# Kernel tuning notes

Hardware: AMD Instinct MI355X
Metric: run time of the kernel (lower is better)

Reference implementation:

```python
import jax, jax.numpy as jnp
import numpy as np

EMBED_DIM = 256
NUM_HEADS = 8
HEAD_DIM = 32
INNER = NUM_HEADS * HEAD_DIM
NEG_SLOPE = 0.2


def setup_inputs() -> dict:
    key = jax.random.key(0)
    ks = jax.random.split(key, 8)
    B, Ns, Nt = 8, 1024, 1024
    src = jax.random.normal(ks[0], (B, Ns, EMBED_DIM), dtype=jnp.float32)
    trg = jax.random.normal(ks[1], (B, Nt, EMBED_DIM), dtype=jnp.float32)
    src_mask = jnp.ones((B, Ns), dtype=bool)
    trg_mask = jax.random.randint(ks[2], (B, Nt), 0, 2).astype(bool)
    # learned params (xavier-ish scale)
    def xavier(k, shape):
        fan_in, fan_out = shape[0], shape[-1]
        lim = (6.0 / (fan_in + fan_out)) ** 0.5
        return jax.random.uniform(k, shape, jnp.float32, -lim, lim)
    W_src = xavier(ks[3], (EMBED_DIM, INNER))
    W_trg = xavier(ks[4], (EMBED_DIM, INNER))  # is_cross_type=True -> independent
    a_src = xavier(ks[5], (NUM_HEADS, HEAD_DIM))
    a_trg = xavier(ks[6], (NUM_HEADS, HEAD_DIM))
    W_out = xavier(ks[7], (INNER, EMBED_DIM))
    return {"src": src, "trg": trg, "src_mask": src_mask, "trg_mask": trg_mask,
            "W_src": W_src, "W_trg": W_trg, "a_src": a_src, "a_trg": a_trg, "W_out": W_out}


def reference(src, trg, src_mask, trg_mask, W_src, W_trg, a_src, a_trg, W_out):
    B, Ns, _ = src.shape
    Nt = trg.shape[1]
    NH, Dh = NUM_HEADS, HEAD_DIM
    src_proj = (src @ W_src).reshape(B, Ns, NH, Dh)  # dropout p=0
    trg_proj = (trg @ W_trg).reshape(B, Nt, NH, Dh)
    score_src = jnp.einsum('bshd,hd->bsh', src_proj, a_src)
    score_trg = jnp.einsum('bthd,hd->bth', trg_proj, a_trg)
    # (B,Ns,NH,1) + (B,1,NH,Nt) -> (B,Ns,NH,Nt)
    scores = score_src[:, :, :, None] + jnp.transpose(score_trg, (0, 2, 1))[:, None, :, :]
    scores = jnp.where(scores >= 0, scores, NEG_SLOPE * scores)  # LeakyReLU
    edge_mask = src_mask[:, :, None, None] & trg_mask[:, None, None, :]
    scores = jnp.where(edge_mask, scores, -jnp.inf)
    attn = jax.nn.softmax(scores, axis=-1)
    attn = jnp.nan_to_num(attn, nan=0.0)
    aggregated = jnp.einsum('bsht,bthd->bshd', attn, trg_proj)
    output = aggregated.reshape(B, Ns, NH * Dh) @ W_out
    return output, jnp.transpose(attn, (0, 2, 1, 3))
```

## Files before the change

### kernel.cpp

```cpp
#include <hip/hip_runtime.h>
#include <hip/hip_bf16.h>
#include <math.h>

#define NB 8
#define NS 1024
#define NT 1024
#define NE 256
#define NHEADS 8
#define DH 32
#define LOG2E 1.4426950408889634f

typedef __attribute__((ext_vector_type(8))) short short8;
typedef __attribute__((ext_vector_type(8))) unsigned short ushort8;
typedef __attribute__((ext_vector_type(4))) float f32x4;

#define O_VT    0u
#define O_WTT   (8u<<20)
#define O_WTO   ((8u<<20)+131072u)
#define O_CSRC  ((8u<<20)+262144u)
#define O_CTRG  (O_CSRC+8192u)
#define O_SSRC  (O_CTRG+8192u)
#define O_STRG  (O_SSRC+262144u)
#define O_FLAG  (O_STRG+262144u)

__device__ __forceinline__ unsigned short f2bf(float f) {
    __hip_bfloat16 h = __float2bfloat16(f);
    union { __hip_bfloat16 h; unsigned short u; } c; c.h = h;
    return c.u;
}
__device__ __forceinline__ float leaky(float v) {
    return (v >= 0.f) ? v : 0.2f * v;
}
__device__ __forceinline__ float exp2_fast(float x) {
    float r;
    asm("v_exp_f32 %0, %1" : "=v"(r) : "v"(x));
    return r;
}

__global__ __launch_bounds__(256) void setup_kernel(
    const unsigned* __restrict__ tmask_dw, const float* __restrict__ Wsrc,
    const float* __restrict__ Wtrg, const float* __restrict__ Wout,
    const float* __restrict__ asrc, const float* __restrict__ atrg,
    float* __restrict__ c_src, float* __restrict__ c_trg,
    unsigned short* __restrict__ Wt_t, unsigned short* __restrict__ Wt_o,
    int* __restrict__ flag) {
    __shared__ __align__(16) char sm[16640];
    const int tid = threadIdx.x;
    const int bid = blockIdx.x;

    if (bid == 0) {
        __shared__ int s_ok;
        if (tid == 0) s_ok = 1;
        __syncthreads();
        for (int i = tid; i < 2048; i += 256)
            if (tmask_dw[i] > 1u) s_ok = 0;
        __syncthreads();
        if (tid == 0) *flag = s_ok;
    } else if (bid <= 2) {
        float* a_sh = (float*)sm;
        const float* W = (bid == 1) ? Wsrc : Wtrg;
        const float* a = (bid == 1) ? asrc : atrg;
        float* c = (bid == 1) ? c_src : c_trg;
        a_sh[tid] = a[tid];
        __syncthreads();
        const int e = tid;
        float ch[8];
#pragma unroll
        for (int h = 0; h < 8; ++h) ch[h] = 0.f;
        for (int i = 0; i < 64; ++i) {
            const float4 wv = *(const float4*)&W[(size_t)e * NE + i * 4];
            const int h = i >> 3, d0 = (i & 7) * 4;
            ch[h] += wv.x * a_sh[h * 32 + d0] + wv.y * a_sh[h * 32 + d0 + 1] +
                     wv.z * a_sh[h * 32 + d0 + 2] + wv.w * a_sh[h * 32 + d0 + 3];
        }
#pragma unroll
        for (int h = 0; h < 8; ++h) c[h * NE + e] = ch[h];
    } else {
        const int q = bid - 3;
        const float* W = (q >> 4) ? Wout : Wtrg;
        unsigned short* Wt = (q >> 4) ? Wt_o : Wt_t;
        const int tl = q & 15;
        const int k0 = (tl >> 2) * 64, n0 = (tl & 3) * 64;
        float* xs = (float*)sm;
#pragma unroll
        for (int it = 0; it < 4; ++it) {
            const int slot = it * 256 + tid;
            const int k = slot >> 4, c4 = slot & 15;
            const float4 v = *(const float4*)&W[(size_t)(k0 + k) * NE + n0 + c4 * 4];
            float* p = &xs[k * 65 + c4 * 4];
            p[0] = v.x; p[1] = v.y; p[2] = v.z; p[3] = v.w;
        }
        __syncthreads();
#pragma unroll
        for (int it = 0; it < 2; ++it) {
            const int slot = it * 256 + tid;
            const int n = slot >> 3, kc = slot & 7;
            ushort8 v;
#pragma unroll
            for (int e = 0; e < 8; ++e)
                v[e] = f2bf(xs[(kc * 8 + e) * 65 + n]);
            *(ushort8*)&Wt[(size_t)(n0 + n) * NE + k0 + kc * 8] = v;
        }
    }
}

__global__ __launch_bounds__(256) void mid_kernel(
    const float* __restrict__ src, const float* __restrict__ trg,
    const float* __restrict__ c_src, const float* __restrict__ c_trg,
    const unsigned short* __restrict__ Wt_t, unsigned short* __restrict__ Vt,
    float* __restrict__ ssrc, float* __restrict__ strg) {
    __shared__ __align__(16) char sm[49152];
    const int tid = threadIdx.x;
    const int bid = blockIdx.x;

    if (bid < 256) {
        unsigned short* As = (unsigned short*)sm;
        unsigned short* ldsT = (unsigned short*)(sm + 32768);
        const int lane = tid & 63, w = tid >> 6;
        const int row0 = (bid >> 1) * 64;
        const int col0 = (bid & 1) * 128;

#pragma unroll
        for (int it = 0; it < 8; ++it) {
            const int gf = it * 256 + tid;
            const int row = gf >> 5, g3 = gf & 31;
            const float4 a = *(const float4*)&trg[(size_t)(row0 + row) * NE + g3 * 8];
            const float4 b = *(const float4*)&trg[(size_t)(row0 + row) * NE + g3 * 8 + 4];
            ushort8 v;
            v[0] = f2bf(a.x); v[1] = f2bf(a.y); v[2] = f2bf(a.z); v[3] = f2bf(a.w);
            v[4] = f2bf(b.x); v[5] = f2bf(b.y); v[6] = f2bf(b.z); v[7] = f2bf(b.w);
            *(ushort8*)&As[row * NE + ((g3 ^ (row & 7)) * 8)] = v;
        }
        __syncthreads();

        const int r = lane & 15, g = lane >> 4;
        short8 af[8];
#pragma unroll
        for (int kk = 0; kk < 8; ++kk)
            af[kk] = *(const short8*)&As[(w * 16 + r) * NE + (((kk * 4 + g) ^ (r & 7)) * 8)];

        f32x4 acc[8];
#pragma unroll
        for (int nt = 0; nt < 8; ++nt) acc[nt] = (f32x4){0.f, 0.f, 0.f, 0.f};
#pragma unroll
        for (int kk = 0; kk < 8; ++kk) {
#pragma unroll
            for (int nt = 0; nt < 8; ++nt) {
                const int col = col0 + nt * 16 + r;
                const short8 bf = *(const short8*)&Wt_t[(size_t)col * NE + kk * 32 + g * 8];
                acc[nt] = __builtin_amdgcn_mfma_f32_16x16x32_bf16(af[kk], bf, acc[nt], 0, 0, 0);
            }
        }
        __syncthreads();

#pragma unroll
        for (int nt = 0; nt < 8; ++nt) {
            const int cl = nt * 16 + r;
            const int sw = (cl & 7) << 3;
#pragma unroll
            for (int j = 0; j < 4; ++j) {
                const int t = w * 16 + g * 4 + j;
                ldsT[cl * 64 + (t ^ sw)] = f2bf(acc[nt][j]);
            }
        }
        __syncthreads();

        const int b = row0 >> 10, t0 = row0 & 1023;
#pragma unroll
        for (int it = 0; it < 4; ++it) {
            const int slot = it * 256 + tid;
            const int cl = slot >> 3, ch = slot & 7;
            const int colg = col0 + cl;
            const int h = colg >> 5, d = colg & 31;
            *(ushort8*)&Vt[(((size_t)(b * 8 + h)) * 32 + d) * 1024 + t0 + ch * 8] =
                *(const ushort8*)&ldsT[cl * 64 + ch * 8];
        }
    } else {
        float* xs = (float*)sm;
        float* cs = (float*)(sm + 32768);
        const int rowg0 = (bid - 256) * 32;
        const bool is_src = rowg0 < NB * NS;
        const float* X = is_src ? (src + (size_t)rowg0 * NE)
                                : (trg + (size_t)(rowg0 - NB * NS) * NE);
        const float* C = is_src ? c_src : c_trg;
        float* S = is_src ? (ssrc + (size_t)rowg0 * NHEADS)
                          : (strg + (size_t)(rowg0 - NB * NS) * NHEADS);

#pragma unroll
        for (int it = 0; it < 8; ++it) {
            const int slot = it * 256 + tid;
            const int row = slot >> 6, c4 = slot & 63;
            *(float4*)&xs[row * NE + c4 * 4] =
                *(const float4*)&X[(size_t)row * NE + c4 * 4];
            cs[slot] = C[slot];
        }
        __syncthreads();

        const int r = tid >> 3, h = tid & 7;
        float s = 0.f;
        for (int e = 0; e < NE; e += 4) {
            const float4 x = *(const float4*)&xs[r * NE + e];
            const float4 c = *(const float4*)&cs[h * NE + e];
            s += x.x * c.x + x.y * c.y + x.z * c.z + x.w * c.w;
        }
        S[(size_t)r * NHEADS + h] = s;
    }
}

__global__ __launch_bounds__(512) void fused_kernel(
    const float* __restrict__ ssrc, const float* __restrict__ strg,
    const void* __restrict__ smask, const void* __restrict__ tmask,
    const int* __restrict__ flag_p, const unsigned short* __restrict__ Vt,
    const unsigned short* __restrict__ Wt_o,
    float* __restrict__ attn, float* __restrict__ out) {
    const int blk = blockIdx.x;
    const int q = blk & 63;
    const int b = blk >> 6;
    const int tid = threadIdx.x;
    const int lane = tid & 63;
    const int w = tid >> 6;
    const int flag = *flag_p;

    __shared__ __align__(16) float s_sm[8][1024];
    __shared__ __align__(16) unsigned short agg_sw[16 * 256];
    __shared__ float s_inv[8][16];

    for (int t = tid; t < NT; t += 512) {
        const bool mv = flag ? (((const int*)tmask)[b * NT + t] != 0)
                             : (((const unsigned char*)tmask)[b * NT + t] != 0);
        const float4 s0 = *(const float4*)&strg[((size_t)b * NT + t) * 8];
        const float4 s1 = *(const float4*)&strg[((size_t)b * NT + t) * 8 + 4];
        const float sv[8] = {s0.x, s0.y, s0.z, s0.w, s1.x, s1.y, s1.z, s1.w};
#pragma unroll
        for (int h = 0; h < 8; ++h)
            s_sm[h][t] = mv ? sv[h] * LOG2E : -1e30f;
    }
    __syncthreads();

    const int r = lane & 15;
    const int g = lane >> 4;
    const int srow = q * 16 + r;
    const bool rowv = flag ? (((const int*)smask)[b * NS + srow] != 0)
                           : (((const unsigned char*)smask)[b * NS + srow] != 0);
    const int sw = (r & 7) << 3;
    const int h = w;
    const float ss2 = ssrc[((size_t)b * NS + srow) * NHEADS + h] * LOG2E;
    const unsigned short* vr0 = Vt + (size_t)(b * 8 + h) * 32768 + r * 1024;
    const unsigned short* vr1 = vr0 + 16 * 1024;

    f32x4 acc0 = {0.f, 0.f, 0.f, 0.f};
    f32x4 acc1 = {0.f, 0.f, 0.f, 0.f};
    float sum = 0.f;
#pragma unroll 4
    for (int c = 0; c < 32; ++c) {
        const int tb = c * 32 + g * 8;
        const short8 b0 = *(const short8*)&vr0[tb ^ sw];
        const short8 b1 = *(const short8*)&vr1[tb ^ sw];
        const float4 v0 = *(const float4*)&s_sm[h][tb];
        const float4 v1 = *(const float4*)&s_sm[h][tb + 4];
        const float vv[8] = {v0.x, v0.y, v0.z, v0.w, v1.x, v1.y, v1.z, v1.w};
        short8 pa;
#pragma unroll
        for (int e = 0; e < 8; ++e) {
            const float p = exp2_fast(leaky(ss2 + vv[e]));
            sum += p;
            pa[e] = (short)f2bf(p);
        }
        acc0 = __builtin_amdgcn_mfma_f32_16x16x32_bf16(pa, b0, acc0, 0, 0, 0);
        acc1 = __builtin_amdgcn_mfma_f32_16x16x32_bf16(pa, b1, acc1, 0, 0, 0);
    }
    sum += __shfl_xor(sum, 16);
    sum += __shfl_xor(sum, 32);
    const float inv = (rowv && sum > 0.f) ? 1.f / sum : 0.f;
    if (g == 0) s_inv[h][r] = inv;
    __syncthreads();

#pragma unroll
    for (int j = 0; j < 4; ++j) {
        const int row = g * 4 + j;
        const float iv = s_inv[h][row];
        int col = h * 32 + r;
        agg_sw[row * 256 + ((((col >> 3) ^ (row & 7)) << 3) | (col & 7))] =
            f2bf(acc0[j] * iv);
        col += 16;
        agg_sw[row * 256 + ((((col >> 3) ^ (row & 7)) << 3) | (col & 7))] =
            f2bf(acc1[j] * iv);
    }
    __syncthreads();

    f32x4 oacc[2];
#pragma unroll
    for (int nt = 0; nt < 2; ++nt) oacc[nt] = (f32x4){0.f, 0.f, 0.f, 0.f};
#pragma unroll
    for (int kk = 0; kk < 8; ++kk) {
        const short8 af = *(const short8*)&agg_sw[r * 256 + (((kk * 4 + g) ^ (r & 7)) * 8)];
#pragma unroll
        for (int nt = 0; nt < 2; ++nt) {
            const int col = w * 32 + nt * 16 + r;
            const short8 bf = *(const short8*)&Wt_o[(size_t)col * NE + kk * 32 + g * 8];
            oacc[nt] = __builtin_amdgcn_mfma_f32_16x16x32_bf16(af, bf, oacc[nt], 0, 0, 0);
        }
    }
#pragma unroll
    for (int nt = 0; nt < 2; ++nt) {
        const int col = w * 32 + nt * 16 + r;
#pragma unroll
        for (int j = 0; j < 4; ++j)
            out[((size_t)b * NS + q * 16 + g * 4 + j) * NE + col] = oacc[nt][j];
    }

    float* wbase = attn + ((size_t)(b * NHEADS + h) * NS + q * 16) * NT;
    for (int rr = 0; rr < 16; ++rr) {
        const float ssr = __shfl(ss2, rr);
        const float ivr = __shfl(inv, rr);
        float* arow = wbase + (size_t)rr * NT;
#pragma unroll
        for (int qq = 0; qq < 4; ++qq) {
            const int t0 = qq * 256 + lane * 4;
            const float4 sm4 = *(const float4*)&s_sm[h][t0];
            float4 o;
            o.x = exp2_fast(leaky(ssr + sm4.x)) * ivr;
            o.y = exp2_fast(leaky(ssr + sm4.y)) * ivr;
            o.z = exp2_fast(leaky(ssr + sm4.z)) * ivr;
            o.w = exp2_fast(leaky(ssr + sm4.w)) * ivr;
            *(float4*)&arow[t0] = o;
        }
    }
}

extern "C" void kernel_launch(void* const* d_in, const int* in_sizes, int n_in,
                              void* d_out, int out_size, void* d_ws, size_t ws_size,
                              hipStream_t stream) {
    const float* src   = (const float*)d_in[0];
    const float* trg   = (const float*)d_in[1];
    const void*  smask = d_in[2];
    const void*  tmask = d_in[3];
    const float* Wsrc  = (const float*)d_in[4];
    const float* Wtrg  = (const float*)d_in[5];
    const float* asrc  = (const float*)d_in[6];
    const float* atrg  = (const float*)d_in[7];
    const float* Wout  = (const float*)d_in[8];

    float* out  = (float*)d_out;
    float* attn = out + (size_t)NB * NS * NE;

    char* wsb = (char*)d_ws;
    unsigned short* Vt   = (unsigned short*)(wsb + O_VT);
    unsigned short* Wt_t = (unsigned short*)(wsb + O_WTT);
    unsigned short* Wt_o = (unsigned short*)(wsb + O_WTO);
    float* c_src = (float*)(wsb + O_CSRC);
    float* c_trg = (float*)(wsb + O_CTRG);
    float* ssrc  = (float*)(wsb + O_SSRC);
    float* strg  = (float*)(wsb + O_STRG);
    int*   flag  = (int*)(wsb + O_FLAG);

    setup_kernel<<<35, 256, 0, stream>>>(
        (const unsigned*)tmask, Wsrc, Wtrg, Wout, asrc, atrg,
        c_src, c_trg, Wt_t, Wt_o, flag);

    mid_kernel<<<768, 256, 0, stream>>>(
        src, trg, c_src, c_trg, Wt_t, Vt, ssrc, strg);

    fused_kernel<<<NB * (NS / 16), 512, 0, stream>>>(
        ssrc, strg, smask, tmask, flag, Vt, Wt_o, attn, out);
}
```

Before: 98.19 us.

## Factor attention exp into per-row and per-column terms and split the attn write kernel

Because exp2(leaky(a+b)) factors as exp2(a)*exp2(b) or exp2(0.2a)*exp2(0.2b), the change precomputes per-target exponentials (masked) in mid_kernel and per-source-row factors (scaled by 1/sum, plus a threshold) in the aggregation kernel. A new attn_kernel then writes the large attention tensor using only multiplies and one compare per element, taking the exp out of the write loop. The attention write also moves out of the fused kernel into its own launch, so the write-bound part runs with a different grid. The cost is an extra launch and workspace traffic, plus possible overflow or precision differences from splitting the exponent.

New measurement: 107.0 us. +9.0%, slower.

```diff
diff --git a/kernel.cpp b/kernel.cpp
--- a/kernel.cpp
+++ b/kernel.cpp
@@ -22,6 +22,8 @@
 #define O_SSRC  (O_CTRG+8192u)
 #define O_STRG  (O_SSRC+262144u)
 #define O_FLAG  (O_STRG+262144u)
+#define O_EST   (12u<<20)
+#define O_RF    (13u<<20)
 
 __device__ __forceinline__ unsigned short f2bf(float f) {
     __hip_bfloat16 h = __float2bfloat16(f);
@@ -108,7 +110,9 @@
     const float* __restrict__ src, const float* __restrict__ trg,
     const float* __restrict__ c_src, const float* __restrict__ c_trg,
     const unsigned short* __restrict__ Wt_t, unsigned short* __restrict__ Vt,
-    float* __restrict__ ssrc, float* __restrict__ strg) {
+    float* __restrict__ ssrc, float* __restrict__ strg,
+    const void* __restrict__ tmask, const int* __restrict__ flag_p,
+    float2* __restrict__ estg) {
     __shared__ __align__(16) char sm[49152];
     const int tid = threadIdx.x;
     const int bid = blockIdx.x;
@@ -204,15 +208,28 @@
             s += x.x * c.x + x.y * c.y + x.z * c.z + x.w * c.w;
         }
         S[(size_t)r * NHEADS + h] = s;
-    }
-}
-
-__global__ __launch_bounds__(512) void fused_kernel(
+
+        if (!is_src) {
+            const int rowg = rowg0 - NB * NS + r;
+            const int flag = *flag_p;
+            const bool mv = flag ? (((const int*)tmask)[rowg] != 0)
+                                 : (((const unsigned char*)tmask)[rowg] != 0);
+            const int bb = rowg >> 10, tt = rowg & 1023;
+            const float s2 = s * LOG2E;
+            float2 e;
+            e.x = mv ? exp2_fast(s2) : 0.f;
+            e.y = mv ? exp2_fast(0.2f * s2) : 0.f;
+            estg[(size_t)(bb * 8 + h) * 1024 + tt] = e;
+        }
+    }
+}
+
+__global__ __launch_bounds__(512) void aggout_kernel(
     const float* __restrict__ ssrc, const float* __restrict__ strg,
     const void* __restrict__ smask, const void* __restrict__ tmask,
     const int* __restrict__ flag_p, const unsigned short* __restrict__ Vt,
     const unsigned short* __restrict__ Wt_o,
-    float* __restrict__ attn, float* __restrict__ out) {
+    float4* __restrict__ rfg, float* __restrict__ out) {
     const int blk = blockIdx.x;
     const int q = blk & 63;
     const int b = blk >> 6;
@@ -272,7 +289,15 @@
     sum += __shfl_xor(sum, 16);
     sum += __shfl_xor(sum, 32);
     const float inv = (rowv && sum > 0.f) ? 1.f / sum : 0.f;
-    if (g == 0) s_inv[h][r] = inv;
+    if (g == 0) {
+        s_inv[h][r] = inv;
+        float4 rf;
+        rf.x = exp2_fast(ss2) * inv;
+        rf.y = exp2_fast(0.2f * ss2) * inv;
+        rf.z = exp2_fast(-ss2);
+        rf.w = 0.f;
+        rfg[(size_t)(b * 8 + h) * 1024 + srow] = rf;
+    }
     __syncthreads();
 
 #pragma unroll
@@ -308,23 +333,29 @@
         for (int j = 0; j < 4; ++j)
             out[((size_t)b * NS + q * 16 + g * 4 + j) * NE + col] = oacc[nt][j];
     }
-
-    float* wbase = attn + ((size_t)(b * NHEADS + h) * NS + q * 16) * NT;
-    for (int rr = 0; rr < 16; ++rr) {
-        const float ssr = __shfl(ss2, rr);
-        const float ivr = __shfl(inv, rr);
-        float* arow = wbase + (size_t)rr * NT;
-#pragma unroll
-        for (int qq = 0; qq < 4; ++qq) {
-            const int t0 = qq * 256 + lane * 4;
-            const float4 sm4 = *(const float4*)&s_sm[h][t0];
-            float4 o;
-            o.x = exp2_fast(leaky(ssr + sm4.x)) * ivr;
-            o.y = exp2_fast(leaky(ssr + sm4.y)) * ivr;
-            o.z = exp2_fast(leaky(ssr + sm4.z)) * ivr;
-            o.w = exp2_fast(leaky(ssr + sm4.w)) * ivr;
-            *(float4*)&arow[t0] = o;
-        }
+}
+
+__global__ __launch_bounds__(256) void attn_kernel(
+    const float4* __restrict__ rfg, const float4* __restrict__ est4,
+    float* __restrict__ attn) {
+    const int blk = blockIdx.x;
+    const int sg = blk & 127, bh = blk >> 7;
+    const int tid = threadIdx.x;
+
+    const float4 p01 = est4[(size_t)bh * 512 + tid * 2];
+    const float4 p23 = est4[(size_t)bh * 512 + tid * 2 + 1];
+    const float4* rfb = rfg + (size_t)bh * 1024 + sg * 8;
+    float* abase = attn + ((size_t)bh * NS + sg * 8) * NT + tid * 4;
+
+#pragma unroll
+    for (int rr = 0; rr < 8; ++rr) {
+        const float4 rf = rfb[rr];
+        float4 o;
+        o.x = (p01.x >= rf.z) ? p01.x * rf.x : p01.y * rf.y;
+        o.y = (p01.z >= rf.z) ? p01.z * rf.x : p01.w * rf.y;
+        o.z = (p23.x >= rf.z) ? p23.x * rf.x : p23.y * rf.y;
+        o.w = (p23.z >= rf.z) ? p23.z * rf.x : p23.w * rf.y;
+        *(float4*)&abase[(size_t)rr * NT] = o;
     }
 }
 
@@ -353,14 +384,19 @@
     float* ssrc  = (float*)(wsb + O_SSRC);
     float* strg  = (float*)(wsb + O_STRG);
     int*   flag  = (int*)(wsb + O_FLAG);
+    float2* estg = (float2*)(wsb + O_EST);
+    float4* rfg  = (float4*)(wsb + O_RF);
 
     setup_kernel<<<35, 256, 0, stream>>>(
         (const unsigned*)tmask, Wsrc, Wtrg, Wout, asrc, atrg,
         c_src, c_trg, Wt_t, Wt_o, flag);
 
     mid_kernel<<<768, 256, 0, stream>>>(
-        src, trg, c_src, c_trg, Wt_t, Vt, ssrc, strg);
-
-    fused_kernel<<<NB * (NS / 16), 512, 0, stream>>>(
-        ssrc, strg, smask, tmask, flag, Vt, Wt_o, attn, out);
-}
+        src, trg, c_src, c_trg, Wt_t, Vt, ssrc, strg, tmask, flag, estg);
+
+    aggout_kernel<<<NB * (NS / 16), 512, 0, stream>>>(
+        ssrc, strg, smask, tmask, flag, Vt, Wt_o, rfg, out);
+
+    attn_kernel<<<64 * 128, 256, 0, stream>>>(
+        rfg, (const float4*)estg, attn);
+}
```
